# Kernel optimization log

Measured on AMD Instinct MI355X. Metric: run time of the kernel, lower is better.

Reference implementation:

```python
import jax, jax.numpy as jnp
import numpy as np

WIN = 7
NUM_HEADS = 4
HEAD_DIM = 32  # 128 / 4


def _relative_position_index(win=WIN):
    coords = np.stack(np.meshgrid(np.arange(win), np.arange(win), indexing='ij'))  # [2,w,w]
    coords = coords.reshape(2, -1)  # [2, w*w]
    rel = coords[:, :, None] - coords[:, None, :]  # [2, ws, ws]
    rel = rel.transpose(1, 2, 0)  # [ws, ws, 2]
    idx = (rel[..., 0] + win - 1) * (2 * win - 1) + (rel[..., 1] + win - 1)
    return jnp.asarray(idx, dtype=jnp.int32)  # [49, 49]


def setup_inputs() -> dict:
    key = jax.random.key(0)
    ks = jax.random.split(key, 6)
    B, S, D = 4096, WIN * WIN, 128
    nW = 64  # windows per image
    return {
        'hidden_states': jax.random.normal(ks[0], (B, S, D), dtype=jnp.float32),
        'attention_mask': jnp.zeros((nW, S, S), dtype=jnp.float32),
        'Wq': jax.random.normal(ks[1], (D, D), dtype=jnp.float32) * 0.02,
        'bq': jnp.zeros((D,), dtype=jnp.float32),
        'Wk': jax.random.normal(ks[2], (D, D), dtype=jnp.float32) * 0.02,
        'bk': jnp.zeros((D,), dtype=jnp.float32),
        'Wv': jax.random.normal(ks[3], (D, D), dtype=jnp.float32) * 0.02,
        'bv': jnp.zeros((D,), dtype=jnp.float32),
        'bias_table': jax.random.normal(ks[4], ((2 * WIN - 1) ** 2, NUM_HEADS), dtype=jnp.float32) * 0.02,
    }


def reference(hidden_states, attention_mask, Wq, bq, Wk, bk, Wv, bv, bias_table):
    B, S, D = hidden_states.shape
    H, Dh = NUM_HEADS, HEAD_DIM

    def heads(x):  # [B,S,D] -> [B,H,S,Dh]
        return x.reshape(B, S, H, Dh).transpose(0, 2, 1, 3)

    q = heads(hidden_states @ Wq + bq)
    k = heads(hidden_states @ Wk + bk)
    v = heads(hidden_states @ Wv + bv)

    scores = jnp.einsum('bhqd,bhkd->bhqk', q, k) / np.sqrt(Dh).astype(np.float32)

    idx = _relative_position_index()  # [S,S] int32 constant
    rel_bias = bias_table[idx]  # [S,S,H]
    scores = scores + rel_bias.transpose(2, 0, 1)[None]  # [B,H,S,S]

    nW = attention_mask.shape[0]
    scores = scores.reshape(B // nW, nW, H, S, S) + attention_mask[None, :, None]
    scores = scores.reshape(B, H, S, S)

    probs = jax.nn.softmax(scores, axis=-1)
    ctx = jnp.einsum('bhqk,bhkd->bhqd', probs, v)
    return ctx.transpose(0, 2, 1, 3).reshape(B, S, D)
```

## Files before the change

### kernel.cpp

```cpp
#include <hip/hip_runtime.h>
#include <hip/hip_bf16.h>

#define S49 49
#define D128 128
#define NH 4
#define VTS 58

typedef __attribute__((ext_vector_type(8))) short short8;
typedef __attribute__((ext_vector_type(4))) unsigned uint4v;
typedef __attribute__((ext_vector_type(4))) float f32x4;

__device__ __forceinline__ unsigned short f2b(float x){
  unsigned u = __builtin_bit_cast(unsigned, x);
  return (unsigned short)((u + 0x7fffu + ((u>>16)&1u)) >> 16);
}
__device__ __forceinline__ unsigned pk2(float a, float b){
  __hip_bfloat162 h = __float22bfloat162_rn(float2{a, b});
  unsigned u; __builtin_memcpy(&u, &h, 4);
  return u;
}
__device__ __forceinline__ int swz256i(int row, int col){
  return row*128 + ((((col>>3) ^ (row&15)) << 3) | (col&7));
}
__device__ __forceinline__ int krow(int nt, int ln){
  return 8*(ln>>2) + (ln&3) + 4*(nt&1) + 32*(nt>>1);
}

__global__ void prep_wt(const float* __restrict__ Wq, const float* __restrict__ Wk,
                        const float* __restrict__ Wv, unsigned short* __restrict__ wt){
  int e = blockIdx.x*256 + threadIdx.x;
  if (e >= 3*128*128) return;
  int mat = e >> 14, rem = e & 16383, n = rem >> 7, k = rem & 127;
  const float* W = (mat==0) ? Wq : ((mat==1) ? Wk : Wv);
  wt[e] = f2b(W[k*128 + n]);
}

__global__ void prep_comb(const float* __restrict__ mask, const float* __restrict__ bt,
                          float4* __restrict__ comb4, int nW){
  int e = blockIdx.x*256 + threadIdx.x;
  if (e >= nW*NH*4*4*64) return;
  int lane = e & 63; int lg = lane >> 4, ln = lane & 15;
  int t = e >> 6;
  int nt = t & 3; t >>= 2;
  int rt = t & 3; t >>= 2;
  int h  = t & (NH-1); int w = t >> 2;
  const int tile = (rt<3) ? rt*16 : 33;
  const int i = tile + ln;
  const float* mrow = mask + ((size_t)w*S49 + i)*S49;
  int ri = i/7, ci = i - ri*7;
  const float L2E = 1.4426950408889634f;
  float v[4];
  #pragma unroll
  for (int r = 0; r < 4; ++r){
    int j = 8*lg + 4*(nt&1) + 32*(nt>>1) + r;
    if (j < S49){
      int rj = j/7, cj = j - rj*7;
      int idx = (ri - rj + 6)*13 + (ci - cj + 6);
      v[r] = (mrow[j] + bt[idx*NH + h]) * L2E;
    } else v[r] = -1e30f;
  }
  float4 o; o.x = v[0]; o.y = v[1]; o.z = v[2]; o.w = v[3];
  comb4[e] = o;
}

__global__ __launch_bounds__(512, 6) void swin_attn(
    const float* __restrict__ hs,
    const float* __restrict__ bq, const float* __restrict__ bk,
    const float* __restrict__ bv,
    const float4* __restrict__ comb4,
    const unsigned short* __restrict__ wt, float* __restrict__ out, int nW){

  __shared__ __align__(16) unsigned short lds[26240];
  unsigned short* hs_s = lds;
  unsigned short* q_s  = lds + 6272;
  unsigned short* k_s  = lds + 12544;
  unsigned short* vt_s = lds + 18816;

  const int b = blockIdx.x;
  const int tid = threadIdx.x;
  const int wave = tid >> 6, lane = tid & 63;
  const int lg = lane >> 4, ln = lane & 15;

  const float* hsb = hs + (size_t)b * (S49*D128);
  #pragma unroll
  for (int it = 0; it < 4; ++it) {
    int u = tid + it*512;
    if (u < S49*32) {
      int row = u >> 5, c = u & 31;
      float4 f = *(const float4*)(hsb + row*128 + c*4);
      uint2 o; o.x = pk2(f.x, f.y); o.y = pk2(f.z, f.w);
      *(uint2*)&hs_s[swz256i(row, c*4)] = o;
    }
  }
  #pragma unroll
  for (int it = 0; it < 2; ++it) {
    int u = tid + it*512;
    if (u < 128*5) {
      int row = u/5, cc = 48 + 2*(u - row*5);
      *(unsigned*)&vt_s[row*VTS + cc] = 0u;
    }
  }
  __syncthreads();

  const int w = b % nW;
  const int rt = wave & 3, hp = wave >> 2;
  const int mbw = (rt<3) ? rt*16 : 33;

  {
    const int ntb = wave*16;
    #pragma unroll 1
    for (int mat = 0; mat < 3; ++mat) {
      short8 a[4];
      #pragma unroll
      for (int ks = 0; ks < 4; ++ks)
        a[ks] = *(const short8*)&wt[(mat<<14) + (ntb+ln)*128 + ks*32 + lg*8];
      const float* bp = (mat==0) ? bq : ((mat==1) ? bk : bv);
      float4 bias = *(const float4*)&bp[ntb + 4*lg];
      #pragma unroll
      for (int mt = 0; mt < 4; ++mt) {
        const int mb = (mt<3) ? mt*16 : 33;
        short8 bh[4];
        #pragma unroll
        for (int ks = 0; ks < 4; ++ks)
          bh[ks] = *(const short8*)&hs_s[swz256i(mb+ln, ks*32 + lg*8)];
        f32x4 acc = {0.f,0.f,0.f,0.f};
        #pragma unroll
        for (int ks = 0; ks < 4; ++ks)
          acc = __builtin_amdgcn_mfma_f32_16x16x32_bf16(a[ks], bh[ks], acc, 0,0,0);
        const int m = mb + ln;
        const int nb = ntb + 4*lg;
        if (mat == 0) {
          uint2 o; o.x = pk2(acc[0]+bias.x, acc[1]+bias.y);
                   o.y = pk2(acc[2]+bias.z, acc[3]+bias.w);
          *(uint2*)&q_s[swz256i(m, nb)] = o;
        } else if (mat == 1) {
          uint2 o; o.x = pk2(acc[0]+bias.x, acc[1]+bias.y);
                   o.y = pk2(acc[2]+bias.z, acc[3]+bias.w);
          *(uint2*)&k_s[swz256i(m, nb)] = o;
        } else {
          vt_s[(nb+0)*VTS + m] = f2b(acc[0]+bias.x);
          vt_s[(nb+1)*VTS + m] = f2b(acc[1]+bias.y);
          vt_s[(nb+2)*VTS + m] = f2b(acc[2]+bias.z);
          vt_s[(nb+3)*VTS + m] = f2b(acc[3]+bias.w);
        }
      }
    }
  }
  __syncthreads();

  const float C1 = 0.17677669529663687f * 1.4426950408889634f;
  const short8 ones = {16256,16256,16256,16256,16256,16256,16256,16256};
  const short8 z8 = {0,0,0,0,0,0,0,0};
  const float4* cbase = comb4 + ((size_t)(w*NH)*4 + rt)*4*64 + lane;

  #pragma unroll
  for (int hh = 0; hh < 2; ++hh) {
    const int h = hp*2 + hh;
    float4 cb[4];
    #pragma unroll
    for (int nt = 0; nt < 4; ++nt)
      cb[nt] = cbase[h*1024 + nt*64];

    short8 aq = *(const short8*)&q_s[swz256i(mbw+ln, h*32 + lg*8)];
    short8 kb[4];
    #pragma unroll
    for (int nt = 0; nt < 4; ++nt)
      kb[nt] = *(const short8*)&k_s[swz256i(krow(nt, ln), h*32 + lg*8)];
    f32x4 st[4];
    __builtin_amdgcn_s_setprio(1);
    #pragma unroll
    for (int nt = 0; nt < 4; ++nt) {
      f32x4 z = {0.f,0.f,0.f,0.f};
      st[nt] = __builtin_amdgcn_mfma_f32_16x16x32_bf16(kb[nt], aq, z, 0,0,0);
    }
    __builtin_amdgcn_s_setprio(0);

    float e[4][4];
    #pragma unroll
    for (int nt = 0; nt < 4; ++nt) {
      float cbv[4] = {cb[nt].x, cb[nt].y, cb[nt].z, cb[nt].w};
      #pragma unroll
      for (int r = 0; r < 4; ++r)
        e[nt][r] = __builtin_amdgcn_exp2f(fmaf(st[nt][r], C1, cbv[r]));
    }

    uint4v u0, u1;
    u0.x = pk2(e[0][0], e[0][1]);
    u0.y = pk2(e[0][2], e[0][3]);
    u0.z = pk2(e[1][0], e[1][1]);
    u0.w = pk2(e[1][2], e[1][3]);
    u1.x = pk2(e[2][0], e[2][1]);
    u1.y = pk2(e[2][2], e[2][3]);
    u1.z = pk2(e[3][0], e[3][1]);
    u1.w = pk2(e[3][2], e[3][3]);
    short8 ap0 = __builtin_bit_cast(short8, u0);
    short8 ap1 = __builtin_bit_cast(short8, u1);

    f32x4 sacc = {0.f,0.f,0.f,0.f};
    __builtin_amdgcn_s_setprio(1);
    sacc = __builtin_amdgcn_mfma_f32_16x16x32_bf16(ap0, ones, sacc, 0,0,0);
    sacc = __builtin_amdgcn_mfma_f32_16x16x32_bf16(ap1, ones, sacc, 0,0,0);
    __builtin_amdgcn_s_setprio(0);

    #pragma unroll
    for (int nt = 0; nt < 2; ++nt) {
      const int vr = h*32 + nt*16 + ln;
      short8 bv0 = *(const short8*)&vt_s[vr*VTS + lg*8];
      short8 bv1 = z8;
      if (lg < 3) bv1 = *(const short8*)&vt_s[vr*VTS + 32 + lg*8];
      f32x4 acc = {0.f,0.f,0.f,0.f};
      __builtin_amdgcn_s_setprio(1);
      acc = __builtin_amdgcn_mfma_f32_16x16x32_bf16(ap0, bv0, acc, 0,0,0);
      acc = __builtin_amdgcn_mfma_f32_16x16x32_bf16(ap1, bv1, acc, 0,0,0);
      __builtin_amdgcn_s_setprio(0);
      const int mr = mbw + 4*lg;
      #pragma unroll
      for (int r = 0; r < 4; ++r)
        out[((size_t)b*S49 + mr + r)*D128 + vr] = acc[r]*__builtin_amdgcn_rcpf(sacc[r]);
    }
  }
}

extern "C" void kernel_launch(void* const* d_in, const int* in_sizes, int n_in,
                              void* d_out, int out_size, void* d_ws, size_t ws_size,
                              hipStream_t stream){
  const float* hs  = (const float*)d_in[0];
  const float* msk = (const float*)d_in[1];
  const float* Wq  = (const float*)d_in[2];
  const float* bq  = (const float*)d_in[3];
  const float* Wk  = (const float*)d_in[4];
  const float* bk  = (const float*)d_in[5];
  const float* Wv  = (const float*)d_in[6];
  const float* bv  = (const float*)d_in[7];
  const float* bt  = (const float*)d_in[8];
  unsigned short* wt = (unsigned short*)d_ws;
  float4* comb4 = (float4*)((char*)d_ws + 98304);
  float* out = (float*)d_out;
  const int B  = in_sizes[0] / (S49*D128);
  const int nW = in_sizes[1] / (S49*S49);
  prep_wt<<<dim3((3*128*128 + 255)/256), dim3(256), 0, stream>>>(Wq, Wk, Wv, wt);
  prep_comb<<<dim3((nW*NH*4*4*64 + 255)/256), dim3(256), 0, stream>>>(msk, bt, comb4, nW);
  swin_attn<<<dim3(B), dim3(512), 0, stream>>>(hs, bq, bk, bv, comb4, wt, out, nW);
}
```

Before: 101.6 us.

## Alias hidden-state LDS buffer with V^T to shrink shared memory

The hidden-state staging buffer now shares LDS with the transposed V buffer. V projection results are held in registers until a barrier and only then written to LDS, which cuts the per-block LDS footprint from about 52KB to 40KB. Launch bounds are raised to 8 waves-per-EU to allow more resident blocks. It adds one extra barrier, register pressure from the held V values, and drops the s_setprio hints around the MFMAs.

```diff
diff --git a/kernel.cpp b/kernel.cpp
--- a/kernel.cpp
+++ b/kernel.cpp
@@ -63,18 +63,18 @@
   comb4[e] = o;
 }
 
-__global__ __launch_bounds__(512, 6) void swin_attn(
+__global__ __launch_bounds__(512, 8) void swin_attn(
     const float* __restrict__ hs,
     const float* __restrict__ bq, const float* __restrict__ bk,
     const float* __restrict__ bv,
     const float4* __restrict__ comb4,
     const unsigned short* __restrict__ wt, float* __restrict__ out, int nW){
 
-  __shared__ __align__(16) unsigned short lds[26240];
-  unsigned short* hs_s = lds;
-  unsigned short* q_s  = lds + 6272;
-  unsigned short* k_s  = lds + 12544;
-  unsigned short* vt_s = lds + 18816;
+  __shared__ __align__(16) unsigned short lds[19968];
+  unsigned short* q_s  = lds;
+  unsigned short* k_s  = lds + 6272;
+  unsigned short* vt_s = lds + 12544;
+  unsigned short* hs_s = vt_s;
 
   const int b = blockIdx.x;
   const int tid = threadIdx.x;
@@ -92,20 +92,13 @@
       *(uint2*)&hs_s[swz256i(row, c*4)] = o;
     }
   }
-  #pragma unroll
-  for (int it = 0; it < 2; ++it) {
-    int u = tid + it*512;
-    if (u < 128*5) {
-      int row = u/5, cc = 48 + 2*(u - row*5);
-      *(unsigned*)&vt_s[row*VTS + cc] = 0u;
-    }
-  }
   __syncthreads();
 
   const int w = b % nW;
   const int rt = wave & 3, hp = wave >> 2;
   const int mbw = (rt<3) ? rt*16 : 33;
 
+  unsigned vreg[4][2];
   {
     const int ntb = wave*16;
     #pragma unroll 1
@@ -138,12 +131,31 @@
                    o.y = pk2(acc[2]+bias.z, acc[3]+bias.w);
           *(uint2*)&k_s[swz256i(m, nb)] = o;
         } else {
-          vt_s[(nb+0)*VTS + m] = f2b(acc[0]+bias.x);
-          vt_s[(nb+1)*VTS + m] = f2b(acc[1]+bias.y);
-          vt_s[(nb+2)*VTS + m] = f2b(acc[2]+bias.z);
-          vt_s[(nb+3)*VTS + m] = f2b(acc[3]+bias.w);
+          vreg[mt][0] = pk2(acc[0]+bias.x, acc[1]+bias.y);
+          vreg[mt][1] = pk2(acc[2]+bias.z, acc[3]+bias.w);
         }
       }
+    }
+  }
+  __syncthreads();
+
+  {
+    const int ntb = wave*16;
+    #pragma unroll
+    for (int mt = 0; mt < 4; ++mt) {
+      const int mb = (mt<3) ? mt*16 : 33;
+      const int m = mb + ln;
+      const int nb = ntb + 4*lg;
+      vt_s[(nb+0)*VTS + m] = (unsigned short)(vreg[mt][0] & 0xffffu);
+      vt_s[(nb+1)*VTS + m] = (unsigned short)(vreg[mt][0] >> 16);
+      vt_s[(nb+2)*VTS + m] = (unsigned short)(vreg[mt][1] & 0xffffu);
+      vt_s[(nb+3)*VTS + m] = (unsigned short)(vreg[mt][1] >> 16);
+    }
+    if (tid < 128) {
+      vt_s[tid*VTS + 49] = 0;
+      *(unsigned*)&vt_s[tid*VTS + 50] = 0u;
+      *(unsigned*)&vt_s[tid*VTS + 52] = 0u;
+      *(unsigned*)&vt_s[tid*VTS + 54] = 0u;
     }
   }
   __syncthreads();
@@ -167,13 +179,11 @@
     for (int nt = 0; nt < 4; ++nt)
       kb[nt] = *(const short8*)&k_s[swz256i(krow(nt, ln), h*32 + lg*8)];
     f32x4 st[4];
-    __builtin_amdgcn_s_setprio(1);
     #pragma unroll
     for (int nt = 0; nt < 4; ++nt) {
       f32x4 z = {0.f,0.f,0.f,0.f};
       st[nt] = __builtin_amdgcn_mfma_f32_16x16x32_bf16(kb[nt], aq, z, 0,0,0);
     }
-    __builtin_amdgcn_s_setprio(0);
 
     float e[4][4];
     #pragma unroll
@@ -197,10 +207,8 @@
     short8 ap1 = __builtin_bit_cast(short8, u1);
 
     f32x4 sacc = {0.f,0.f,0.f,0.f};
-    __builtin_amdgcn_s_setprio(1);
     sacc = __builtin_amdgcn_mfma_f32_16x16x32_bf16(ap0, ones, sacc, 0,0,0);
     sacc = __builtin_amdgcn_mfma_f32_16x16x32_bf16(ap1, ones, sacc, 0,0,0);
-    __builtin_amdgcn_s_setprio(0);
 
     #pragma unroll
     for (int nt = 0; nt < 2; ++nt) {
@@ -209,10 +217,8 @@
       short8 bv1 = z8;
       if (lg < 3) bv1 = *(const short8*)&vt_s[vr*VTS + 32 + lg*8];
       f32x4 acc = {0.f,0.f,0.f,0.f};
-      __builtin_amdgcn_s_setprio(1);
       acc = __builtin_amdgcn_mfma_f32_16x16x32_bf16(ap0, bv0, acc, 0,0,0);
       acc = __builtin_amdgcn_mfma_f32_16x16x32_bf16(ap1, bv1, acc, 0,0,0);
-      __builtin_amdgcn_s_setprio(0);
       const int mr = mbw + 4*lg;
       #pragma unroll
       for (int r = 0; r < 4; ++r)
```

After: 141.6 us. +39.5%, slower.
